# Kernel optimization log

Hardware: AMD Instinct MI355X
Metric: run time of the kernel (lower is better)

## Reference

```python
import jax, jax.numpy as jnp
import numpy as np

B, N = 256, 65536          # batch, num_tokens (world.num_tokens == N)
VOCAB = 50257
ALPHA = 0.5                # dirichlet concentration
EPS = 1e-7                 # gumbel eps


def setup_inputs() -> dict:
    key = jax.random.key(0)
    kb, kt, ku, kd = jax.random.split(key, 4)
    batch = jax.random.randint(kb, (B, N), 0, VOCAB, dtype=jnp.int32)
    t = jax.random.uniform(kt, (B,), dtype=jnp.float32)
    U = jax.random.uniform(ku, (B, N), dtype=jnp.float32)
    # dirichlet(alpha=0.5) sample over the token axis, one simplex per row
    D = jax.random.dirichlet(kd, ALPHA * jnp.ones((N,), jnp.float32), shape=(B,)).astype(jnp.float32)
    return {"batch": batch, "t": t, "U": U, "D": D}


def cosine_schedule(t):
    return 1.0 - jnp.cos(jnp.pi * t / 2)


def cosine_weight(t, eps=1e-3):
    t_adj = t * (1 - 2 * eps) + eps
    return 0.5 * jnp.pi * jnp.sin(jnp.pi * t_adj / 2)


def binary_topk(weights, ks):
    # weights: [B, N] float; ks: [B, 1] int -> bool mask marking the top-k per row
    Bn, Nn = weights.shape
    idx = jnp.argsort(-weights, axis=-1)                     # descending order indices
    rank = jnp.broadcast_to(jnp.arange(Nn), (Bn, Nn))        # rank of each sorted slot
    mask = jnp.zeros((Bn, Nn), dtype=bool)
    mask = mask.at[jnp.arange(Bn)[:, None], idx].set(ks > rank)
    return mask


def reference(batch, t, U, D):
    r = cosine_schedule(t)                                   # mask rate per sample [B]
    w = cosine_weight(t)                                     # loss weight per sample [B]
    G = -jnp.log(-jnp.log(U + EPS) + EPS)                    # gumbel noise [B, N]
    weights = G + jnp.log(D)                                 # gumbel + log-dirichlet
    ks = (N * r).astype(jnp.int32)[:, None]                  # [B, 1] tokens to mask
    mask = binary_topk(weights, ks)                          # [B, N] bool
    return mask, w
```

## Files before the change

kernel.cpp:

```cpp
#include <hip/hip_runtime.h>
#include <math.h>

#define BB 256
#define NN 65536
#define NT 1024
#define CAP 2016
#define MARGIN 2e-3f
#define NLC 7

typedef float f32x4 __attribute__((ext_vector_type(4)));

__device__ __forceinline__ unsigned int f2sort(float f) {
    unsigned int b = __float_as_uint(f);
    return (b & 0x80000000u) ? ~b : (b | 0x80000000u);
}
__device__ __forceinline__ float sort2f(unsigned int u) {
    unsigned int b = (u & 0x80000000u) ? (u & 0x7fffffffu) : ~u;
    return __uint_as_float(b);
}

__device__ __forceinline__ unsigned int wexact(float u, float d) {
    float t1 = u + 1e-7f;
    float t2 = (float)log((double)t1);
    float t3 = (-t2) + 1e-7f;
    float G  = -(float)log((double)t3);
    float lgD = (float)log((double)d);
    return f2sort(G + lgD);
}

__device__ __forceinline__ unsigned int wfast(float u, float d) {
    float t1 = u + 1e-7f;
    float t3 = -__logf(t1) + 1e-7f;
    float G  = -__logf(t3);
    return f2sort(G + __logf(d));
}

__device__ __forceinline__ bool finite_f(float f) {
    return (__float_as_uint(f) & 0x7f800000u) != 0x7f800000u;
}

#define PASS1SEL(KKV) \
    { const int b0 = tid * 8; unsigned int cs = 0; \
      _Pragma("unroll") for (int i = 0; i < 8; i++) cs += hist[b0 + i]; \
      chunkSum[tid] = cs; } \
    __syncthreads(); \
    if (tid < 64) { \
        const int c0i = lane * 16; unsigned int s = 0; \
        _Pragma("unroll") for (int i = 0; i < 16; i++) s += chunkSum[c0i + i]; \
        unsigned int suf = s; \
        _Pragma("unroll") for (int off = 1; off < 64; off <<= 1) { \
            unsigned int tv = __shfl_down(suf, off); if (lane + off < 64) suf += tv; } \
        unsigned int above = suf - s; \
        if (suf >= (KKV) && above < (KKV)) { \
            unsigned int cum = above; \
            for (int ci = c0i + 15; ci >= c0i; ci--) { \
                unsigned int cch = chunkSum[ci]; \
                if (cum + cch >= (KKV)) { \
                    for (int b = ci * 8 + 7; ; b--) { \
                        unsigned int c2 = hist[b]; \
                        if (cum + c2 >= (KKV)) { s_sel = (unsigned int)b; s_kneed = (KKV) - cum; s_eq = c2; break; } \
                        cum += c2; } \
                    break; } \
                cum += cch; } } } \
    __syncthreads();

#define PASS2SEL(P, KN) \
    if (tid < 64) { \
        const int c0i = lane * 16; unsigned int s = 0; \
        _Pragma("unroll") for (int i = 0; i < 16; i++) s += hist[c0i + i]; \
        unsigned int suf = s; \
        _Pragma("unroll") for (int off = 1; off < 64; off <<= 1) { \
            unsigned int tv = __shfl_down(suf, off); if (lane + off < 64) suf += tv; } \
        unsigned int above = suf - s; \
        if (suf >= (KN) && above < (KN)) { \
            unsigned int cum = above; \
            for (int b = c0i + 15; ; b--) { \
                unsigned int c2 = hist[b]; \
                if (cum + c2 >= (KN)) { s_sel = ((P) << 10) | (unsigned int)b; s_kneed = (KN) - cum; s_eq = c2; break; } \
                cum += c2; } } } \
    __syncthreads();

#define PASS3SEL(P, KN) \
    if (tid < 64) { \
        const int c0i = lane * 8; unsigned int s = 0; \
        _Pragma("unroll") for (int i = 0; i < 8; i++) s += hist[c0i + i]; \
        unsigned int suf = s; \
        _Pragma("unroll") for (int off = 1; off < 64; off <<= 1) { \
            unsigned int tv = __shfl_down(suf, off); if (lane + off < 64) suf += tv; } \
        unsigned int above = suf - s; \
        if (suf >= (KN) && above < (KN)) { \
            unsigned int cum = above; \
            for (int b = c0i + 7; ; b--) { \
                unsigned int c2 = hist[b]; \
                if (cum + c2 >= (KN)) { s_sel = ((P) << 9) | (unsigned int)b; s_kneed = (KN) - cum; s_eq = c2; break; } \
                cum += c2; } } } \
    __syncthreads();

__global__ __launch_bounds__(NT, 4)
void md_fused_kernel(const float* __restrict__ Tt,
                     const float* __restrict__ U,
                     const float* __restrict__ D,
                     float* __restrict__ out,
                     float* __restrict__ wout) {
    const int row = blockIdx.x;
    const int tid = threadIdx.x;
    const int lane = tid & 63;

    const float* Ur = U + (size_t)row * NN;
    const float* Dr = D + (size_t)row * NN;
    float* Or = out + (size_t)row * NN;

    __shared__ uint4 kls[NLC * 1024];
    __shared__ unsigned int hist[8192];
    __shared__ unsigned int chunkSum[NT];
    __shared__ int bandIdx[CAP];
    __shared__ unsigned int s_sel, s_kneed, s_eq;
    __shared__ int s_A, s_bandCnt, s_tiecnt, s_tieidx;

    unsigned int* bandU = (unsigned int*)kls;
    int* tielist = bandIdx;

    const float t = Tt[row];
    const float pf = (float)M_PI;
    float aa = pf * t;
    float bbv = aa * 0.5f;
    float c0 = (float)cos((double)bbv);
    float r  = 1.0f - c0;
    const int k = (int)(65536.0f * r);
    if (tid == 0) {
        float tadj = t * 0.998f + 0.001f;
        float arg  = (pf * tadj) * 0.5f;
        wout[row] = (float)(0.5 * M_PI) * (float)sin((double)arg);
    }

    if (k <= 0 || k >= NN) {
        const float fill = (k >= NN) ? 1.0f : 0.0f;
        f32x4 f4 = {fill, fill, fill, fill};
        for (int j = 0; j < 16; j++)
            __builtin_nontemporal_store(f4, (f32x4*)(Or + j * 4096 + tid * 4));
        return;
    }
    const unsigned int kk = (unsigned int)k;

    for (int i = tid; i < 8192; i += NT) hist[i] = 0;
    if (tid == 0) { s_A = 0; s_bandCnt = 0; }
    __syncthreads();

#pragma unroll 2
    for (int J = 0; J < 16; ++J) {
        const int e = (J << 12) + (tid << 2);
        float4 u4 = *(const float4*)(Ur + e);
        float4 d4 = *(const float4*)(Dr + e);
        uint4 kv;
        kv.x = wfast(u4.x, d4.x);
        kv.y = wfast(u4.y, d4.y);
        kv.z = wfast(u4.z, d4.z);
        kv.w = wfast(u4.w, d4.w);
        if (J < NLC) kls[(J << 10) + tid] = kv;
        atomicAdd(&hist[kv.x >> 19], 1u);
        atomicAdd(&hist[kv.y >> 19], 1u);
        atomicAdd(&hist[kv.z >> 19], 1u);
        atomicAdd(&hist[kv.w >> 19], 1u);
    }
    __syncthreads();

    PASS1SEL(kk)
    const unsigned int p13 = s_sel;
    const unsigned int kn1 = s_kneed;
    hist[tid] = 0;
    __syncthreads();

#pragma unroll 2
    for (int J = 0; J < 16; ++J) {
        uint4 kv;
        if (J < NLC) {
            kv = kls[(J << 10) + tid];
        } else {
            const int e = (J << 12) + (tid << 2);
            float4 u4 = *(const float4*)(Ur + e);
            float4 d4 = *(const float4*)(Dr + e);
            kv.x = wfast(u4.x, d4.x);
            kv.y = wfast(u4.y, d4.y);
            kv.z = wfast(u4.z, d4.z);
            kv.w = wfast(u4.w, d4.w);
        }
        if ((kv.x >> 19) == p13) atomicAdd(&hist[(kv.x >> 9) & 1023u], 1u);
        if ((kv.y >> 19) == p13) atomicAdd(&hist[(kv.y >> 9) & 1023u], 1u);
        if ((kv.z >> 19) == p13) atomicAdd(&hist[(kv.z >> 9) & 1023u], 1u);
        if ((kv.w >> 19) == p13) atomicAdd(&hist[(kv.w >> 9) & 1023u], 1u);
    }
    __syncthreads();
    PASS2SEL(p13, kn1)

    const unsigned int p23 = s_sel;
    const float loF = sort2f(p23 << 9) - MARGIN;
    const float hiF = sort2f((p23 << 9) | 511u) + MARGIN;
    const bool badBand = !(finite_f(loF) && finite_f(hiF));
    const unsigned int lo_u = f2sort(loF);
    const unsigned int hi_u = f2sort(hiF);

    {
        int cnt = 0;
#pragma unroll 2
        for (int J = 0; J < 16; ++J) {
            const int e = (J << 12) + (tid << 2);
            uint4 kv;
            if (J < NLC) {
                kv = kls[(J << 10) + tid];
            } else {
                float4 u4 = *(const float4*)(Ur + e);
                float4 d4 = *(const float4*)(Dr + e);
                kv.x = wfast(u4.x, d4.x);
                kv.y = wfast(u4.y, d4.y);
                kv.z = wfast(u4.z, d4.z);
                kv.w = wfast(u4.w, d4.w);
            }
            f32x4 m;
#define MRGV(UU, EIDX, MF) { const unsigned int uu = (UU); \
            const bool din = uu > hi_u; cnt += (int)din; MF = din ? 1.0f : 0.0f; \
            if (!din && uu >= lo_u) { \
                int slot = atomicAdd(&s_bandCnt, 1); \
                if (slot < CAP) bandIdx[slot] = (EIDX); } }
            MRGV(kv.x, e + 0, m.x)
            MRGV(kv.y, e + 1, m.y)
            MRGV(kv.z, e + 2, m.z)
            MRGV(kv.w, e + 3, m.w)
#undef MRGV
            __builtin_nontemporal_store(m, (f32x4*)(Or + e));
        }
#pragma unroll
        for (int off = 32; off >= 1; off >>= 1) cnt += __shfl_down(cnt, off);
        if (lane == 0) atomicAdd(&s_A, cnt);
    }
    __syncthreads();

    const int bandCnt = s_bandCnt;
    const int kb = k - s_A;
    const bool fallback = badBand || (bandCnt > CAP) || (kb < 0) || (kb > bandCnt);

    if (!fallback) {
        for (int j = tid; j < bandCnt; j += NT) {
            int idx = bandIdx[j];
            bandU[j] = wexact(Ur[idx], Dr[idx]);
        }
        __syncthreads();
        for (int j = tid; j < bandCnt; j += NT) {
            unsigned int me = bandU[j];
            int mi = bandIdx[j];
            int rk = 0;
            for (int i = 0; i < bandCnt; i++) {
                unsigned int o = bandU[i];
                rk += (int)((o > me) || (o == me && bandIdx[i] < mi));
            }
            if (rk < kb) Or[mi] = 1.0f;
        }
        return;
    }

    __syncthreads();
    for (int i = tid; i < 8192; i += NT) hist[i] = 0;
    __syncthreads();
#pragma unroll 1
    for (int J = 0; J < 16; ++J) {
        const int e = (J << 12) + (tid << 2);
        float4 u4 = *(const float4*)(Ur + e);
        float4 d4 = *(const float4*)(Dr + e);
        uint4 kv;
        kv.x = wexact(u4.x, d4.x);
        kv.y = wexact(u4.y, d4.y);
        kv.z = wexact(u4.z, d4.z);
        kv.w = wexact(u4.w, d4.w);
        if (J < NLC) kls[(J << 10) + tid] = kv;
        atomicAdd(&hist[kv.x >> 19], 1u);
        atomicAdd(&hist[kv.y >> 19], 1u);
        atomicAdd(&hist[kv.z >> 19], 1u);
        atomicAdd(&hist[kv.w >> 19], 1u);
    }
    __syncthreads();

    PASS1SEL(kk)
    const unsigned int q13 = s_sel;
    const unsigned int en1 = s_kneed;
    hist[tid] = 0;
    __syncthreads();
#pragma unroll 1
    for (int J = 0; J < 16; ++J) {
        uint4 kv;
        if (J < NLC) {
            kv = kls[(J << 10) + tid];
        } else {
            const int e = (J << 12) + (tid << 2);
            float4 u4 = *(const float4*)(Ur + e);
            float4 d4 = *(const float4*)(Dr + e);
            kv.x = wexact(u4.x, d4.x);
            kv.y = wexact(u4.y, d4.y);
            kv.z = wexact(u4.z, d4.z);
            kv.w = wexact(u4.w, d4.w);
        }
        if ((kv.x >> 19) == q13) atomicAdd(&hist[(kv.x >> 9) & 1023u], 1u);
        if ((kv.y >> 19) == q13) atomicAdd(&hist[(kv.y >> 9) & 1023u], 1u);
        if ((kv.z >> 19) == q13) atomicAdd(&hist[(kv.z >> 9) & 1023u], 1u);
        if ((kv.w >> 19) == q13) atomicAdd(&hist[(kv.w >> 9) & 1023u], 1u);
    }
    __syncthreads();
    PASS2SEL(q13, en1)

    const unsigned int q23 = s_sel;
    const unsigned int en2 = s_kneed;
    if (tid < 512) hist[tid] = 0;
    __syncthreads();
#pragma unroll 1
    for (int J = 0; J < 16; ++J) {
        uint4 kv;
        if (J < NLC) {
            kv = kls[(J << 10) + tid];
        } else {
            const int e = (J << 12) + (tid << 2);
            float4 u4 = *(const float4*)(Ur + e);
            float4 d4 = *(const float4*)(Dr + e);
            kv.x = wexact(u4.x, d4.x);
            kv.y = wexact(u4.y, d4.y);
            kv.z = wexact(u4.z, d4.z);
            kv.w = wexact(u4.w, d4.w);
        }
        if ((kv.x >> 9) == q23) atomicAdd(&hist[kv.x & 511u], 1u);
        if ((kv.y >> 9) == q23) atomicAdd(&hist[kv.y & 511u], 1u);
        if ((kv.z >> 9) == q23) atomicAdd(&hist[kv.z & 511u], 1u);
        if ((kv.w >> 9) == q23) atomicAdd(&hist[kv.w & 511u], 1u);
    }
    __syncthreads();
    PASS3SEL(q23, en2)

    const unsigned int theta = s_sel;
    const unsigned int kneedF = s_kneed, eqF = s_eq;
    const bool needOrder = (kneedF < eqF);
    int istar = NN;
    if (needOrder) {
        if (tid == 0) s_tiecnt = 0;
        __syncthreads();
#pragma unroll 1
        for (int J = 0; J < 16; ++J) {
            const int e = (J << 12) + (tid << 2);
            uint4 kv;
            if (J < NLC) {
                kv = kls[(J << 10) + tid];
            } else {
                float4 u4 = *(const float4*)(Ur + e);
                float4 d4 = *(const float4*)(Dr + e);
                kv.x = wexact(u4.x, d4.x);
                kv.y = wexact(u4.y, d4.y);
                kv.z = wexact(u4.z, d4.z);
                kv.w = wexact(u4.w, d4.w);
            }
#define TIEV(UU, EIDX) if ((UU) == theta) { \
                int pos = atomicAdd(&s_tiecnt, 1); \
                if (pos < 1024) tielist[pos] = (EIDX); }
            TIEV(kv.x, e + 0)
            TIEV(kv.y, e + 1)
            TIEV(kv.z, e + 2)
            TIEV(kv.w, e + 3)
#undef TIEV
        }
        __syncthreads();
        if (tid == 0) {
            int E = s_tiecnt; if (E > 1024) E = 1024;
            for (int aI = 1; aI < E; aI++) {
                int val = tielist[aI]; int bI = aI - 1;
                while (bI >= 0 && tielist[bI] > val) { tielist[bI + 1] = tielist[bI]; bI--; }
                tielist[bI + 1] = val;
            }
            int kk2 = (int)kneedF; if (kk2 > E) kk2 = E; if (kk2 < 1) kk2 = 1;
            s_tieidx = tielist[kk2 - 1];
        }
        __syncthreads();
        istar = s_tieidx;
    }

#pragma unroll 1
    for (int J = 0; J < 16; ++J) {
        const int e = (J << 12) + (tid << 2);
        uint4 kv;
        if (J < NLC) {
            kv = kls[(J << 10) + tid];
        } else {
            float4 u4 = *(const float4*)(Ur + e);
            float4 d4 = *(const float4*)(Dr + e);
            kv.x = wexact(u4.x, d4.x);
            kv.y = wexact(u4.y, d4.y);
            kv.z = wexact(u4.z, d4.z);
            kv.w = wexact(u4.w, d4.w);
        }
        f32x4 m;
#define MVE(u, idx) ((((u) > theta) || ((u) == theta && (!needOrder || (idx) <= istar))) ? 1.0f : 0.0f)
        m.x = MVE(kv.x, e + 0);
        m.y = MVE(kv.y, e + 1);
        m.z = MVE(kv.z, e + 2);
        m.w = MVE(kv.w, e + 3);
#undef MVE
        __builtin_nontemporal_store(m, (f32x4*)(Or + e));
    }
}

extern "C" void kernel_launch(void* const* d_in, const int* in_sizes, int n_in,
                              void* d_out, int out_size, void* d_ws, size_t ws_size,
                              hipStream_t stream) {
    const float* T = (const float*)d_in[1];
    const float* U = (const float*)d_in[2];
    const float* D = (const float*)d_in[3];
    float* out = (float*)d_out;
    float* wout = out + (size_t)BB * NN;

    md_fused_kernel<<<BB, NT, 0, stream>>>(T, U, D, out, wout);
}
```

Measured before the change: 241.5 us.

## Stage sort keys in the output buffer instead of LDS cache plus recompute

The first pass now writes every computed sort key into the row's slice of the output buffer. Later passes reread those keys from global memory, which should mostly hit L2, instead of keeping only 7 of 16 chunks in LDS and reloading U/D and recomputing the Gumbel key for the rest. Dropping the large LDS cache also shrinks shared memory per block, which may allow more blocks per CU. In exchange it adds global write and read traffic for the keys, and the mask is stored as raw bit patterns over the staged keys.

```diff
diff --git a/kernel.cpp b/kernel.cpp
--- a/kernel.cpp
+++ b/kernel.cpp
@@ -6,9 +6,11 @@
 #define NT 1024
 #define CAP 2016
 #define MARGIN 2e-3f
-#define NLC 7
 
 typedef float f32x4 __attribute__((ext_vector_type(4)));
+typedef unsigned int u32x4 __attribute__((ext_vector_type(4)));
+
+#define ONE_BITS 0x3F800000u
 
 __device__ __forceinline__ unsigned int f2sort(float f) {
     unsigned int b = __float_as_uint(f);
@@ -108,16 +110,15 @@
 
     const float* Ur = U + (size_t)row * NN;
     const float* Dr = D + (size_t)row * NN;
-    float* Or = out + (size_t)row * NN;
-
-    __shared__ uint4 kls[NLC * 1024];
+    unsigned int* OrU = (unsigned int*)out + (size_t)row * NN;
+
     __shared__ unsigned int hist[8192];
     __shared__ unsigned int chunkSum[NT];
+    __shared__ unsigned int bandU[CAP];
     __shared__ int bandIdx[CAP];
     __shared__ unsigned int s_sel, s_kneed, s_eq;
     __shared__ int s_A, s_bandCnt, s_tiecnt, s_tieidx;
 
-    unsigned int* bandU = (unsigned int*)kls;
     int* tielist = bandIdx;
 
     const float t = Tt[row];
@@ -134,10 +135,10 @@
     }
 
     if (k <= 0 || k >= NN) {
-        const float fill = (k >= NN) ? 1.0f : 0.0f;
-        f32x4 f4 = {fill, fill, fill, fill};
+        const unsigned int fb = (k >= NN) ? ONE_BITS : 0u;
+        u32x4 f4 = {fb, fb, fb, fb};
         for (int j = 0; j < 16; j++)
-            __builtin_nontemporal_store(f4, (f32x4*)(Or + j * 4096 + tid * 4));
+            __builtin_nontemporal_store(f4, (u32x4*)(OrU + j * 4096 + tid * 4));
         return;
     }
     const unsigned int kk = (unsigned int)k;
@@ -151,12 +152,12 @@
         const int e = (J << 12) + (tid << 2);
         float4 u4 = *(const float4*)(Ur + e);
         float4 d4 = *(const float4*)(Dr + e);
-        uint4 kv;
+        u32x4 kv;
         kv.x = wfast(u4.x, d4.x);
         kv.y = wfast(u4.y, d4.y);
         kv.z = wfast(u4.z, d4.z);
         kv.w = wfast(u4.w, d4.w);
-        if (J < NLC) kls[(J << 10) + tid] = kv;
+        *(u32x4*)(OrU + e) = kv;
         atomicAdd(&hist[kv.x >> 19], 1u);
         atomicAdd(&hist[kv.y >> 19], 1u);
         atomicAdd(&hist[kv.z >> 19], 1u);
@@ -172,18 +173,8 @@
 
 #pragma unroll 2
     for (int J = 0; J < 16; ++J) {
-        uint4 kv;
-        if (J < NLC) {
-            kv = kls[(J << 10) + tid];
-        } else {
-            const int e = (J << 12) + (tid << 2);
-            float4 u4 = *(const float4*)(Ur + e);
-            float4 d4 = *(const float4*)(Dr + e);
-            kv.x = wfast(u4.x, d4.x);
-            kv.y = wfast(u4.y, d4.y);
-            kv.z = wfast(u4.z, d4.z);
-            kv.w = wfast(u4.w, d4.w);
-        }
+        const int e = (J << 12) + (tid << 2);
+        u32x4 kv = *(const u32x4*)(OrU + e);
         if ((kv.x >> 19) == p13) atomicAdd(&hist[(kv.x >> 9) & 1023u], 1u);
         if ((kv.y >> 19) == p13) atomicAdd(&hist[(kv.y >> 9) & 1023u], 1u);
         if ((kv.z >> 19) == p13) atomicAdd(&hist[(kv.z >> 9) & 1023u], 1u);
@@ -204,20 +195,10 @@
 #pragma unroll 2
         for (int J = 0; J < 16; ++J) {
             const int e = (J << 12) + (tid << 2);
-            uint4 kv;
-            if (J < NLC) {
-                kv = kls[(J << 10) + tid];
-            } else {
-                float4 u4 = *(const float4*)(Ur + e);
-                float4 d4 = *(const float4*)(Dr + e);
-                kv.x = wfast(u4.x, d4.x);
-                kv.y = wfast(u4.y, d4.y);
-                kv.z = wfast(u4.z, d4.z);
-                kv.w = wfast(u4.w, d4.w);
-            }
-            f32x4 m;
+            u32x4 kv = __builtin_nontemporal_load((const u32x4*)(OrU + e));
+            u32x4 m;
 #define MRGV(UU, EIDX, MF) { const unsigned int uu = (UU); \
-            const bool din = uu > hi_u; cnt += (int)din; MF = din ? 1.0f : 0.0f; \
+            const bool din = uu > hi_u; cnt += (int)din; MF = din ? ONE_BITS : 0u; \
             if (!din && uu >= lo_u) { \
                 int slot = atomicAdd(&s_bandCnt, 1); \
                 if (slot < CAP) bandIdx[slot] = (EIDX); } }
@@ -226,7 +207,7 @@
             MRGV(kv.z, e + 2, m.z)
             MRGV(kv.w, e + 3, m.w)
 #undef MRGV
-            __builtin_nontemporal_store(m, (f32x4*)(Or + e));
+            __builtin_nontemporal_store(m, (u32x4*)(OrU + e));
         }
 #pragma unroll
         for (int off = 32; off >= 1; off >>= 1) cnt += __shfl_down(cnt, off);
@@ -252,7 +233,7 @@
                 unsigned int o = bandU[i];
                 rk += (int)((o > me) || (o == me && bandIdx[i] < mi));
             }
-            if (rk < kb) Or[mi] = 1.0f;
+            if (rk < kb) OrU[mi] = ONE_BITS;
         }
         return;
     }
@@ -265,12 +246,12 @@
         const int e = (J << 12) + (tid << 2);
         float4 u4 = *(const float4*)(Ur + e);
         float4 d4 = *(const float4*)(Dr + e);
-        uint4 kv;
+        u32x4 kv;
         kv.x = wexact(u4.x, d4.x);
         kv.y = wexact(u4.y, d4.y);
         kv.z = wexact(u4.z, d4.z);
         kv.w = wexact(u4.w, d4.w);
-        if (J < NLC) kls[(J << 10) + tid] = kv;
+        *(u32x4*)(OrU + e) = kv;
         atomicAdd(&hist[kv.x >> 19], 1u);
         atomicAdd(&hist[kv.y >> 19], 1u);
         atomicAdd(&hist[kv.z >> 19], 1u);
@@ -285,18 +266,8 @@
     __syncthreads();
 #pragma unroll 1
     for (int J = 0; J < 16; ++J) {
-        uint4 kv;
-        if (J < NLC) {
-            kv = kls[(J << 10) + tid];
-        } else {
-            const int e = (J << 12) + (tid << 2);
-            float4 u4 = *(const float4*)(Ur + e);
-            float4 d4 = *(const float4*)(Dr + e);
-            kv.x = wexact(u4.x, d4.x);
-            kv.y = wexact(u4.y, d4.y);
-            kv.z = wexact(u4.z, d4.z);
-            kv.w = wexact(u4.w, d4.w);
-        }
+        const int e = (J << 12) + (tid << 2);
+        u32x4 kv = *(const u32x4*)(OrU + e);
         if ((kv.x >> 19) == q13) atomicAdd(&hist[(kv.x >> 9) & 1023u], 1u);
         if ((kv.y >> 19) == q13) atomicAdd(&hist[(kv.y >> 9) & 1023u], 1u);
         if ((kv.z >> 19) == q13) atomicAdd(&hist[(kv.z >> 9) & 1023u], 1u);
@@ -311,18 +282,8 @@
     __syncthreads();
 #pragma unroll 1
     for (int J = 0; J < 16; ++J) {
-        uint4 kv;
-        if (J < NLC) {
-            kv = kls[(J << 10) + tid];
-        } else {
-            const int e = (J << 12) + (tid << 2);
-            float4 u4 = *(const float4*)(Ur + e);
-            float4 d4 = *(const float4*)(Dr + e);
-            kv.x = wexact(u4.x, d4.x);
-            kv.y = wexact(u4.y, d4.y);
-            kv.z = wexact(u4.z, d4.z);
-            kv.w = wexact(u4.w, d4.w);
-        }
+        const int e = (J << 12) + (tid << 2);
+        u32x4 kv = *(const u32x4*)(OrU + e);
         if ((kv.x >> 9) == q23) atomicAdd(&hist[kv.x & 511u], 1u);
         if ((kv.y >> 9) == q23) atomicAdd(&hist[kv.y & 511u], 1u);
         if ((kv.z >> 9) == q23) atomicAdd(&hist[kv.z & 511u], 1u);
@@ -341,17 +302,7 @@
 #pragma unroll 1
         for (int J = 0; J < 16; ++J) {
             const int e = (J << 12) + (tid << 2);
-            uint4 kv;
-            if (J < NLC) {
-                kv = kls[(J << 10) + tid];
-            } else {
-                float4 u4 = *(const float4*)(Ur + e);
-                float4 d4 = *(const float4*)(Dr + e);
-                kv.x = wexact(u4.x, d4.x);
-                kv.y = wexact(u4.y, d4.y);
-                kv.z = wexact(u4.z, d4.z);
-                kv.w = wexact(u4.w, d4.w);
-            }
+            u32x4 kv = *(const u32x4*)(OrU + e);
 #define TIEV(UU, EIDX) if ((UU) == theta) { \
                 int pos = atomicAdd(&s_tiecnt, 1); \
                 if (pos < 1024) tielist[pos] = (EIDX); }
@@ -379,25 +330,15 @@
 #pragma unroll 1
     for (int J = 0; J < 16; ++J) {
         const int e = (J << 12) + (tid << 2);
-        uint4 kv;
-        if (J < NLC) {
-            kv = kls[(J << 10) + tid];
-        } else {
-            float4 u4 = *(const float4*)(Ur + e);
-            float4 d4 = *(const float4*)(Dr + e);
-            kv.x = wexact(u4.x, d4.x);
-            kv.y = wexact(u4.y, d4.y);
-            kv.z = wexact(u4.z, d4.z);
-            kv.w = wexact(u4.w, d4.w);
-        }
-        f32x4 m;
-#define MVE(u, idx) ((((u) > theta) || ((u) == theta && (!needOrder || (idx) <= istar))) ? 1.0f : 0.0f)
+        u32x4 kv = __builtin_nontemporal_load((const u32x4*)(OrU + e));
+        u32x4 m;
+#define MVE(u, idx) ((((u) > theta) || ((u) == theta && (!needOrder || (idx) <= istar))) ? ONE_BITS : 0u)
         m.x = MVE(kv.x, e + 0);
         m.y = MVE(kv.y, e + 1);
         m.z = MVE(kv.z, e + 2);
         m.w = MVE(kv.w, e + 3);
 #undef MVE
-        __builtin_nontemporal_store(m, (f32x4*)(Or + e));
+        __builtin_nontemporal_store(m, (u32x4*)(OrU + e));
     }
 }
 
```

Result: faster. 233.5 us (-3.3%).
